# Performance work log

Hardware: AMD Instinct MI355X
Metric: run time of the kernel (lower is better)

Reference implementation:

```python
import jax, jax.numpy as jnp
import numpy as np

N_NODES = 100000
N_EDGES = 1200000
NFEAT = 64
NHID = 64
NCLASS = 16
BN_EPS = 1e-5
L2_EPS = 1e-12


def setup_inputs() -> dict:
    key = jax.random.key(0)
    ks = jax.random.split(key, 8)
    edge_index = jax.random.randint(ks[0], (2, N_EDGES), 0, N_NODES, dtype=jnp.int64)
    x = jax.random.normal(ks[1], (N_NODES, NFEAT), dtype=jnp.float32)
    # SAGEConv params: lin_l (neighbor path, has bias), lin_r (root path, no bias)
    W_l = jax.random.normal(ks[2], (NHID, NFEAT), dtype=jnp.float32) * (1.0 / np.sqrt(NFEAT))
    b_l = jnp.zeros((NHID,), dtype=jnp.float32)
    W_r = jax.random.normal(ks[3], (NHID, NFEAT), dtype=jnp.float32) * (1.0 / np.sqrt(NFEAT))
    # BatchNorm1d affine params
    gamma = jnp.ones((NHID,), dtype=jnp.float32)
    beta = jnp.zeros((NHID,), dtype=jnp.float32)
    # final fc (xavier-ish scale, zero bias per weights_init)
    W_fc = jax.random.normal(ks[4], (NCLASS, NHID), dtype=jnp.float32) * (1.0 / np.sqrt(NHID))
    b_fc = jnp.zeros((NCLASS,), dtype=jnp.float32)
    return {"edge_index": edge_index, "x": x, "W_l": W_l, "b_l": b_l,
            "W_r": W_r, "gamma": gamma, "beta": beta, "W_fc": W_fc, "b_fc": b_fc}


def reference(edge_index, x, W_l, b_l, W_r, gamma, beta, W_fc, b_fc):
    N = x.shape[0]
    src, dst = edge_index[0], edge_index[1]
    # SAGEConv mean aggregation: gather x at source nodes, scatter-mean to dst
    msgs = x[src]                                                  # [E, F]
    sums = jax.ops.segment_sum(msgs, dst, num_segments=N)         # [N, F]
    cnt = jax.ops.segment_sum(jnp.ones((src.shape[0], 1), x.dtype), dst, num_segments=N)
    mean = sums / jnp.maximum(cnt, 1.0)
    # out = lin_l(mean_neighbors) + lin_r(x_root)
    h = mean @ W_l.T + b_l + x @ W_r.T                              # [N, H]
    # normalize=True -> L2 normalize rows (F.normalize semantics)
    h = h / jnp.maximum(jnp.linalg.norm(h, axis=-1, keepdims=True), L2_EPS)
    # transition: ReLU -> BatchNorm1d (training stats) -> Dropout (identity in eval)
    h = jax.nn.relu(h)
    mu = jnp.mean(h, axis=0)
    var = jnp.var(h, axis=0)
    h = (h - mu) / jnp.sqrt(var + BN_EPS) * gamma + beta
    return h @ W_fc.T + b_fc                                        # [N, C]
```

## Files before the change

### kernel.cpp

```cpp
#include <hip/hip_runtime.h>
#include <hip/hip_bf16.h>


typedef __attribute__((ext_vector_type(8))) short short8;
typedef __attribute__((ext_vector_type(4))) float f32x4;

__device__ __forceinline__ unsigned short f2bf(float f) {
    unsigned int u = __builtin_bit_cast(unsigned int, f);
    u += 0x7FFFu + ((u >> 16) & 1u);
    return (unsigned short)(u >> 16);
}
__device__ __forceinline__ float bf2f(unsigned short s) {
    return __builtin_bit_cast(float, ((unsigned int)s) << 16);
}

#define CHUNK 8192

__device__ __forceinline__ int exclScan256(int v, int* swv) {
    const int t = threadIdx.x, lane = t & 63, wid = t >> 6;
    __syncthreads();
    int s = v;
#pragma unroll
    for (int off = 1; off < 64; off <<= 1) {
        int tt = __shfl_up(s, off);
        if (lane >= off) s += tt;
    }
    if (lane == 63) swv[wid] = s;
    __syncthreads();
    if (t == 0) {
        int a = 0;
#pragma unroll
        for (int w = 0; w < 4; ++w) { int tt = swv[w]; swv[w] = a; a += tt; }
    }
    __syncthreads();
    return s - v + swv[wid];
}

__global__ __launch_bounds__(256) void k_prep(const int* __restrict__ eidx,
                                              int* __restrict__ cnt,
                                              const float4* __restrict__ x4,
                                              ushort4* __restrict__ xbf,
                                              int E, int NB, int NBLK,
                                              int n4, int do_x) {
    __shared__ int lh[256];
    const int tid = threadIdx.x;
    if ((int)blockIdx.x < NBLK) {
        lh[tid] = 0;
        __syncthreads();
        const int base = blockIdx.x * CHUNK;
        for (int i = tid; i < CHUNK; i += 256) {
            int e = base + i;
            if (e < E) atomicAdd(&lh[eidx[E + e] >> 9], 1);
        }
        __syncthreads();
        if (tid < NB) cnt[(size_t)tid * NBLK + blockIdx.x] = lh[tid];
    } else if (do_x) {
        int t = ((int)blockIdx.x - NBLK) * 256 + tid;
        if (t < n4) {
            float4 v = x4[t];
            xbf[t] = make_ushort4(f2bf(v.x), f2bf(v.y), f2bf(v.z), f2bf(v.w));
        }
    }
}

__global__ __launch_bounds__(256) void k_scanbkt(int* __restrict__ cnt,
                                                 int* __restrict__ btot,
                                                 int NBLK) {
    __shared__ int swv[4];
    const int b = blockIdx.x;
    const int t = threadIdx.x;
    int v = (t < NBLK) ? cnt[(size_t)b * NBLK + t] : 0;
    int excl = exclScan256(v, swv);
    if (t < NBLK) cnt[(size_t)b * NBLK + t] = excl;
    if (t == 255) btot[b] = excl + v;
}

__global__ __launch_bounds__(256) void k_bscatter(const int* __restrict__ eidx,
                                                  const int* __restrict__ cnt,
                                                  const int* __restrict__ btot,
                                                  unsigned int* __restrict__ ebuf,
                                                  int E, int NB, int NBLK) {
    __shared__ int cur[256];
    __shared__ int swv[4];
    const int tid = threadIdx.x;
    int bv = (tid < NB) ? btot[tid] : 0;
    int bexcl = exclScan256(bv, swv);
    if (tid < NB)
        cur[tid] = bexcl + cnt[(size_t)tid * NBLK + blockIdx.x];
    __syncthreads();
    const int base = blockIdx.x * CHUNK;
    for (int i = tid; i < CHUNK; i += 256) {
        int e = base + i;
        if (e < E) {
            int d = eidx[E + e];
            int s = eidx[e];
            int p = atomicAdd(&cur[d >> 9], 1);
            ebuf[p] = (unsigned int)s | ((unsigned int)(d & 511) << 17);
        }
    }
}

__global__ __launch_bounds__(256) void k_bfinal(const unsigned int* __restrict__ ebuf,
                                                const int* __restrict__ btot,
                                                int* __restrict__ rowptr,
                                                int* __restrict__ colv,
                                                int N, int NB, int E) {
    __shared__ int h[512];
    __shared__ int swv[4];
    __shared__ int sseg[2];
    const int b = blockIdx.x;
    const int tid = threadIdx.x;
    int bv = (tid < NB) ? btot[tid] : 0;
    int bexcl = exclScan256(bv, swv);
    if (tid == b) { sseg[0] = bexcl; sseg[1] = bexcl + bv; }
    h[2 * tid] = 0;
    h[2 * tid + 1] = 0;
    __syncthreads();
    const int segb = sseg[0], sege = sseg[1];
    for (int i = segb + tid; i < sege; i += 256)
        atomicAdd(&h[ebuf[i] >> 17], 1);
    __syncthreads();
    int a0 = h[2 * tid], a1 = h[2 * tid + 1];
    int ts = a0 + a1;
    const int lane = tid & 63, wid = tid >> 6;
    int s = ts;
#pragma unroll
    for (int off = 1; off < 64; off <<= 1) {
        int tt = __shfl_up(s, off);
        if (lane >= off) s += tt;
    }
    if (lane == 63) swv[wid] = s;
    __syncthreads();
    if (tid == 0) {
        int a = 0;
#pragma unroll
        for (int w = 0; w < 4; ++w) { int tt = swv[w]; swv[w] = a; a += tt; }
    }
    __syncthreads();
    int excl = s - ts + swv[wid];
    h[2 * tid] = excl;
    h[2 * tid + 1] = excl + a0;
    int node = b * 512 + 2 * tid;
    if (node < N) rowptr[node] = segb + excl;
    if (node + 1 < N) rowptr[node + 1] = segb + excl + a0;
    __syncthreads();
    for (int i = segb + tid; i < sege; i += 256) {
        unsigned int u = ebuf[i];
        int p = atomicAdd(&h[u >> 17], 1);
        colv[segb + p] = (int)(u & 0x1FFFFu);
    }
    if (b == 0 && tid == 0) rowptr[N] = E;
}

__global__ __launch_bounds__(256) void k_gfused(
        const unsigned short* __restrict__ xbf,
        const int* __restrict__ rowptr, const int* __restrict__ colv,
        const float* __restrict__ Wl, const float* __restrict__ bl,
        const float* __restrict__ Wr,
        unsigned short* __restrict__ mh,
        float* __restrict__ pstats, int N) {
    __shared__ unsigned short sm[16][72];

    const int tid = threadIdx.x;
    const int tbase = blockIdx.x * 16;

    {
        const int nloc = tid >> 4;
        const int l = tid & 15;
        const int mrow = tbase + nloc;
        const int mld = (mrow < N) ? mrow : (N - 1);
        const uint2* xbf2 = (const uint2*)xbf;
        int b = rowptr[mld], e = rowptr[mld + 1];
        float a0 = 0.f, a1 = 0.f, a2 = 0.f, a3 = 0.f;
        int p = b;
        for (; p + 4 <= e; p += 4) {
            int s0 = colv[p], s1 = colv[p + 1], s2 = colv[p + 2], s3 = colv[p + 3];
            uint2 v0 = xbf2[(size_t)s0 * 16 + l];
            uint2 v1 = xbf2[(size_t)s1 * 16 + l];
            uint2 v2 = xbf2[(size_t)s2 * 16 + l];
            uint2 v3 = xbf2[(size_t)s3 * 16 + l];
            a0 += bf2f((unsigned short)(v0.x & 0xFFFF)) + bf2f((unsigned short)(v1.x & 0xFFFF)) +
                  bf2f((unsigned short)(v2.x & 0xFFFF)) + bf2f((unsigned short)(v3.x & 0xFFFF));
            a1 += bf2f((unsigned short)(v0.x >> 16)) + bf2f((unsigned short)(v1.x >> 16)) +
                  bf2f((unsigned short)(v2.x >> 16)) + bf2f((unsigned short)(v3.x >> 16));
            a2 += bf2f((unsigned short)(v0.y & 0xFFFF)) + bf2f((unsigned short)(v1.y & 0xFFFF)) +
                  bf2f((unsigned short)(v2.y & 0xFFFF)) + bf2f((unsigned short)(v3.y & 0xFFFF));
            a3 += bf2f((unsigned short)(v0.y >> 16)) + bf2f((unsigned short)(v1.y >> 16)) +
                  bf2f((unsigned short)(v2.y >> 16)) + bf2f((unsigned short)(v3.y >> 16));
        }
        for (; p < e; ++p) {
            int s0 = colv[p];
            uint2 v0 = xbf2[(size_t)s0 * 16 + l];
            a0 += bf2f((unsigned short)(v0.x & 0xFFFF));
            a1 += bf2f((unsigned short)(v0.x >> 16));
            a2 += bf2f((unsigned short)(v0.y & 0xFFFF));
            a3 += bf2f((unsigned short)(v0.y >> 16));
        }
        float inv = 1.0f / fmaxf((float)(e - b), 1.0f);
        *(ushort4*)&sm[nloc][l * 4] = make_ushort4(f2bf(a0 * inv), f2bf(a1 * inv),
                                                   f2bf(a2 * inv), f2bf(a3 * inv));
    }
    __syncthreads();
    if (tid >= 64) return;

    const int lane = tid;
    const int l15 = lane & 15;
    const int quad = lane >> 4;

    short8 afr[2], rfr[2];
    afr[0] = *(const short8*)&sm[l15][quad * 8];
    afr[1] = *(const short8*)&sm[l15][32 + quad * 8];
    const int rrow = tbase + l15;
    const int rld = (rrow < N) ? rrow : (N - 1);
    rfr[0] = *(const short8*)(xbf + (size_t)rld * 64 + quad * 8);
    rfr[1] = *(const short8*)(xbf + (size_t)rld * 64 + 32 + quad * 8);

    float blv[4];
#pragma unroll
    for (int f = 0; f < 4; ++f) blv[f] = bl[f * 16 + l15];

    f32x4 acc[4] = {{0.f, 0.f, 0.f, 0.f}, {0.f, 0.f, 0.f, 0.f},
                    {0.f, 0.f, 0.f, 0.f}, {0.f, 0.f, 0.f, 0.f}};
#pragma unroll
    for (int c = 0; c < 4; ++c) {
#pragma unroll
        for (int f = 0; f < 4; ++f) {
            const int n = f * 16 + l15;
            const float* wsrc = (c < 2)
                ? (Wl + (size_t)n * 64 + c * 32 + quad * 8)
                : (Wr + (size_t)n * 64 + (c - 2) * 32 + quad * 8);
            float4 w0 = *(const float4*)wsrc;
            float4 w1 = *(const float4*)(wsrc + 4);
            union { short8 v; unsigned short u[8]; } pk;
            pk.u[0] = f2bf(w0.x); pk.u[1] = f2bf(w0.y);
            pk.u[2] = f2bf(w0.z); pk.u[3] = f2bf(w0.w);
            pk.u[4] = f2bf(w1.x); pk.u[5] = f2bf(w1.y);
            pk.u[6] = f2bf(w1.z); pk.u[7] = f2bf(w1.w);
            acc[f] = __builtin_amdgcn_mfma_f32_16x16x32_bf16(
                (c < 2) ? afr[c] : rfr[c - 2], pk.v, acc[f], 0, 0, 0);
        }
    }

    float psum[4] = {0.f, 0.f, 0.f, 0.f};
    float psq[4] = {0.f, 0.f, 0.f, 0.f};
#pragma unroll
    for (int reg = 0; reg < 4; ++reg) {
        const int node = tbase + quad * 4 + reg;
        float hv[4];
        float ss = 0.f;
#pragma unroll
        for (int f = 0; f < 4; ++f) {
            hv[f] = acc[f][reg] + blv[f];
            ss += hv[f] * hv[f];
        }
        ss += __shfl_xor(ss, 1);
        ss += __shfl_xor(ss, 2);
        ss += __shfl_xor(ss, 4);
        ss += __shfl_xor(ss, 8);
        float sc = 1.0f / fmaxf(sqrtf(ss), 1e-12f);
        if (node < N) {
#pragma unroll
            for (int f = 0; f < 4; ++f) {
                float r = fmaxf(hv[f] * sc, 0.f);
                unsigned short rb = f2bf(r);
                float e = bf2f(rb);
                mh[(size_t)node * 64 + f * 16 + l15] = rb;
                psum[f] += e;
                psq[f] += e * e;
            }
        }
    }

#pragma unroll
    for (int f = 0; f < 4; ++f) {
        psum[f] += __shfl_xor(psum[f], 16);
        psum[f] += __shfl_xor(psum[f], 32);
        psq[f] += __shfl_xor(psq[f], 16);
        psq[f] += __shfl_xor(psq[f], 32);
    }
    if (lane < 16) {
#pragma unroll
        for (int f = 0; f < 4; ++f) {
            pstats[(size_t)blockIdx.x * 128 + f * 16 + l15] = psum[f];
            pstats[(size_t)blockIdx.x * 128 + 64 + f * 16 + l15] = psq[f];
        }
    }
}

__global__ __launch_bounds__(256) void k_gather_f32(
        const float4* __restrict__ x4, const int* __restrict__ rowptr,
        const int* __restrict__ colv, ushort4* __restrict__ mh, int N) {
    int t = blockIdx.x * 256 + threadIdx.x;
    int n = t >> 4;
    int l = t & 15;
    if (n >= N) return;
    int b = rowptr[n], e = rowptr[n + 1];
    float ax = 0.f, ay = 0.f, az = 0.f, aw = 0.f;
    int p = b;
    for (; p + 4 <= e; p += 4) {
        int s0 = colv[p], s1 = colv[p + 1], s2 = colv[p + 2], s3 = colv[p + 3];
        float4 v0 = x4[(size_t)s0 * 16 + l];
        float4 v1 = x4[(size_t)s1 * 16 + l];
        float4 v2 = x4[(size_t)s2 * 16 + l];
        float4 v3 = x4[(size_t)s3 * 16 + l];
        ax += (v0.x + v1.x) + (v2.x + v3.x);
        ay += (v0.y + v1.y) + (v2.y + v3.y);
        az += (v0.z + v1.z) + (v2.z + v3.z);
        aw += (v0.w + v1.w) + (v2.w + v3.w);
    }
    for (; p < e; ++p) {
        int s0 = colv[p];
        float4 v0 = x4[(size_t)s0 * 16 + l];
        ax += v0.x; ay += v0.y; az += v0.z; aw += v0.w;
    }
    float inv = 1.0f / fmaxf((float)(e - b), 1.0f);
    mh[(size_t)n * 16 + l] = make_ushort4(f2bf(ax * inv), f2bf(ay * inv),
                                          f2bf(az * inv), f2bf(aw * inv));
}

__global__ __launch_bounds__(256) void k_fused_legacy(
        const float* __restrict__ x,
        const float* __restrict__ Wl, const float* __restrict__ bl,
        const float* __restrict__ Wr,
        unsigned short* __restrict__ mh,
        float* __restrict__ pstats, int N) {
    __shared__ float sRed[4][128];
    const int tid = threadIdx.x;
    const int wid = tid >> 6;
    const int lane = tid & 63;
    const int l15 = lane & 15;
    const int quad = lane >> 4;

    short8 bfrag[4][4];
#pragma unroll
    for (int c = 0; c < 4; ++c) {
#pragma unroll
        for (int f = 0; f < 4; ++f) {
            const int n = f * 16 + l15;
            const float* wsrc = (c < 2)
                ? (Wl + (size_t)n * 64 + c * 32 + quad * 8)
                : (Wr + (size_t)n * 64 + (c - 2) * 32 + quad * 8);
            float4 w0 = *(const float4*)wsrc;
            float4 w1 = *(const float4*)(wsrc + 4);
            union { short8 v; unsigned short u[8]; } pk;
            pk.u[0] = f2bf(w0.x); pk.u[1] = f2bf(w0.y);
            pk.u[2] = f2bf(w0.z); pk.u[3] = f2bf(w0.w);
            pk.u[4] = f2bf(w1.x); pk.u[5] = f2bf(w1.y);
            pk.u[6] = f2bf(w1.z); pk.u[7] = f2bf(w1.w);
            bfrag[c][f] = pk.v;
        }
    }
    float blv[4];
#pragma unroll
    for (int f = 0; f < 4; ++f) blv[f] = bl[f * 16 + l15];

    const int tbase = blockIdx.x * 64 + wid * 16;
    const int mrow = tbase + l15;
    const int mld = (mrow < N) ? mrow : (N - 1);
    f32x4 acc[4] = {{0.f, 0.f, 0.f, 0.f}, {0.f, 0.f, 0.f, 0.f},
                    {0.f, 0.f, 0.f, 0.f}, {0.f, 0.f, 0.f, 0.f}};
#pragma unroll
    for (int c = 0; c < 2; ++c) {
        short8 a = *(const short8*)(mh + (size_t)mld * 64 + c * 32 + quad * 8);
#pragma unroll
        for (int f = 0; f < 4; ++f)
            acc[f] = __builtin_amdgcn_mfma_f32_16x16x32_bf16(a, bfrag[c][f], acc[f], 0, 0, 0);
    }
#pragma unroll
    for (int c = 0; c < 2; ++c) {
        const float* xp = x + (size_t)mld * 64 + c * 32 + quad * 8;
        float4 a0 = *(const float4*)xp;
        float4 a1 = *(const float4*)(xp + 4);
        union { short8 v; unsigned short u[8]; } pk;
        pk.u[0] = f2bf(a0.x); pk.u[1] = f2bf(a0.y);
        pk.u[2] = f2bf(a0.z); pk.u[3] = f2bf(a0.w);
        pk.u[4] = f2bf(a1.x); pk.u[5] = f2bf(a1.y);
        pk.u[6] = f2bf(a1.z); pk.u[7] = f2bf(a1.w);
#pragma unroll
        for (int f = 0; f < 4; ++f)
            acc[f] = __builtin_amdgcn_mfma_f32_16x16x32_bf16(pk.v, bfrag[c + 2][f], acc[f], 0, 0, 0);
    }

    float psum[4] = {0.f, 0.f, 0.f, 0.f};
    float psq[4] = {0.f, 0.f, 0.f, 0.f};
#pragma unroll
    for (int reg = 0; reg < 4; ++reg) {
        const int node = tbase + quad * 4 + reg;
        float hv[4];
        float ss = 0.f;
#pragma unroll
        for (int f = 0; f < 4; ++f) {
            hv[f] = acc[f][reg] + blv[f];
            ss += hv[f] * hv[f];
        }
        ss += __shfl_xor(ss, 1);
        ss += __shfl_xor(ss, 2);
        ss += __shfl_xor(ss, 4);
        ss += __shfl_xor(ss, 8);
        float sc = 1.0f / fmaxf(sqrtf(ss), 1e-12f);
        if (node < N) {
#pragma unroll
            for (int f = 0; f < 4; ++f) {
                float r = fmaxf(hv[f] * sc, 0.f);
                unsigned short rb = f2bf(r);
                float e = bf2f(rb);
                mh[(size_t)node * 64 + f * 16 + l15] = rb;
                psum[f] += e;
                psq[f] += e * e;
            }
        }
    }
#pragma unroll
    for (int f = 0; f < 4; ++f) {
        psum[f] += __shfl_xor(psum[f], 16);
        psum[f] += __shfl_xor(psum[f], 32);
        psq[f] += __shfl_xor(psq[f], 16);
        psq[f] += __shfl_xor(psq[f], 32);
    }
    if (lane < 16) {
#pragma unroll
        for (int f = 0; f < 4; ++f) {
            sRed[wid][f * 16 + l15] = psum[f];
            sRed[wid][64 + f * 16 + l15] = psq[f];
        }
    }
    __syncthreads();
    if (tid < 128) {
        float v = sRed[0][tid] + sRed[1][tid] + sRed[2][tid] + sRed[3][tid];
        pstats[(size_t)blockIdx.x * 128 + tid] = v;
    }
}

__global__ __launch_bounds__(64) void k_stats(const float* __restrict__ pstats,
                                              float* __restrict__ stats, int nblk) {
    int col = blockIdx.x;
    int l = threadIdx.x;
    float s = 0.f;
    for (int r = l; r < nblk; r += 64) s += pstats[(size_t)r * 128 + col];
    s += __shfl_xor(s, 1);
    s += __shfl_xor(s, 2);
    s += __shfl_xor(s, 4);
    s += __shfl_xor(s, 8);
    s += __shfl_xor(s, 16);
    s += __shfl_xor(s, 32);
    if (l == 0) stats[col] = s;
}

__global__ __launch_bounds__(256) void k_out(
        const unsigned short* __restrict__ h, const float* __restrict__ stats,
        const float* __restrict__ gamma, const float* __restrict__ beta,
        const float* __restrict__ Wfc, const float* __restrict__ bfc,
        float* __restrict__ out, int N) {
    __shared__ float sWm[64 * 16];
    __shared__ float sShift[64];
    __shared__ float sBase[16];
    const int tid = threadIdx.x;
    const float invN = 1.0f / (float)N;
    if (tid < 64) {
        float mu = stats[tid] * invN;
        float var = stats[64 + tid] * invN - mu * mu;
        float sc = gamma[tid] / sqrtf(var + 1e-5f);
        sShift[tid] = beta[tid] - mu * sc;
#pragma unroll
        for (int c = 0; c < 16; ++c) sWm[tid * 16 + c] = Wfc[c * 64 + tid] * sc;
    }
    __syncthreads();
    if (tid < 16) {
        float b = bfc[tid];
#pragma unroll
        for (int j = 0; j < 64; ++j) b += sShift[j] * Wfc[tid * 64 + j];
        sBase[tid] = b;
    }
    __syncthreads();
    int g = blockIdx.x * 256 + tid;
    int n = g >> 4;
    int c = g & 15;
    if (n >= N) return;
    const ushort4* h4 = (const ushort4*)(h + (size_t)n * 64);
    float acc = sBase[c];
#pragma unroll
    for (int jq = 0; jq < 16; ++jq) {
        ushort4 v = h4[jq];
        acc += bf2f(v.x) * sWm[(jq * 4 + 0) * 16 + c];
        acc += bf2f(v.y) * sWm[(jq * 4 + 1) * 16 + c];
        acc += bf2f(v.z) * sWm[(jq * 4 + 2) * 16 + c];
        acc += bf2f(v.w) * sWm[(jq * 4 + 3) * 16 + c];
    }
    out[(size_t)n * 16 + c] = acc;
}

extern "C" void kernel_launch(void* const* d_in, const int* in_sizes, int n_in,
                              void* d_out, int out_size, void* d_ws, size_t ws_size,
                              hipStream_t stream) {
    const int* eidx = (const int*)d_in[0];
    const float* x = (const float*)d_in[1];
    const float* Wl = (const float*)d_in[2];
    const float* bl = (const float*)d_in[3];
    const float* Wr = (const float*)d_in[4];
    const float* gamma = (const float*)d_in[5];
    const float* beta = (const float*)d_in[6];
    const float* Wfc = (const float*)d_in[7];
    const float* bfc = (const float*)d_in[8];
    float* out = (float*)d_out;

    const int E = in_sizes[0] / 2;
    const int N = in_sizes[1] / 64;
    const int NB = (N + 511) >> 9;
    const int NBLK = (E + CHUNK - 1) / CHUNK;
    const int fbG = (N + 15) / 16;
    const int fbL = (N + 63) / 64;
    const int n4 = N * 16;

    int* cnt = (int*)d_ws;
    int* btot = cnt + (size_t)NB * NBLK;
    int* rowptr = btot + NB;
    float* pstats = (float*)(rowptr + N + 1);
    float* stats = pstats + (size_t)fbG * 128;
    int* colv = (int*)(stats + 128);
    unsigned int* ebuf = (unsigned int*)(colv + E);
    unsigned short* mh = (unsigned short*)(((uintptr_t)(ebuf + E) + 15) & ~(uintptr_t)15);
    unsigned short* xbf = mh + (size_t)N * 64;

    size_t need_bf = (size_t)((char*)(xbf + (size_t)N * 64) - (char*)d_ws);
    const int use_bf = (ws_size >= need_bf) ? 1 : 0;

    int cbl = use_bf ? (n4 + 255) / 256 : 0;
    k_prep<<<NBLK + cbl, 256, 0, stream>>>(eidx, cnt, (const float4*)x,
                                           (ushort4*)xbf, E, NB, NBLK, n4, use_bf);
    k_scanbkt<<<NB, 256, 0, stream>>>(cnt, btot, NBLK);
    k_bscatter<<<NBLK, 256, 0, stream>>>(eidx, cnt, btot, ebuf, E, NB, NBLK);
    k_bfinal<<<NB, 256, 0, stream>>>(ebuf, btot, rowptr, colv, N, NB, E);

    if (use_bf) {
        k_gfused<<<fbG, 256, 0, stream>>>(xbf, rowptr, colv, Wl, bl, Wr,
                                          mh, pstats, N);
        k_stats<<<128, 64, 0, stream>>>(pstats, stats, fbG);
    } else {
        int gblocks = (int)(((size_t)N * 16 + 255) / 256);
        k_gather_f32<<<gblocks, 256, 0, stream>>>((const float4*)x, rowptr, colv,
                                                  (ushort4*)mh, N);
        k_fused_legacy<<<fbL, 256, 0, stream>>>(x, Wl, bl, Wr, mh, pstats, N);
        k_stats<<<128, 64, 0, stream>>>(pstats, stats, fbL);
    }

    int oblocks = (int)(((size_t)N * 16 + 255) / 256);
    k_out<<<oblocks, 256, 0, stream>>>(mh, stats, gamma, beta, Wfc, bfc, out, N);
}
```

Before: 245.3 us.

## Split fused GEMM epilogue across all four wavefronts by output column tile

The MFMA projection stage after the neighbor gather previously ran on a single wavefront, leaving three of four waves idle. Each wave now computes one 16-column tile of the 64-wide output. The per-row L2 norm is assembled through a small shared-memory buffer and an extra barrier, and BN partial stats are written per column. This spreads weight conversion and MFMA work across the block, in exchange for a block-wide sync and redundant loads of the A fragments by every wave.

```diff
diff --git a/kernel.cpp b/kernel.cpp
--- a/kernel.cpp
+++ b/kernel.cpp
@@ -160,6 +160,7 @@
         unsigned short* __restrict__ mh,
         float* __restrict__ pstats, int N) {
     __shared__ unsigned short sm[16][72];
+    __shared__ float ssS[16][4];
 
     const int tid = threadIdx.x;
     const int tbase = blockIdx.x * 16;
@@ -201,11 +202,12 @@
                                                    f2bf(a2 * inv), f2bf(a3 * inv));
     }
     __syncthreads();
-    if (tid >= 64) return;
-
-    const int lane = tid;
+
+    const int wid = tid >> 6;
+    const int lane = tid & 63;
     const int l15 = lane & 15;
     const int quad = lane >> 4;
+    const int n = wid * 16 + l15;
 
     short8 afr[2], rfr[2];
     afr[0] = *(const short8*)&sm[l15][quad * 8];
@@ -215,75 +217,61 @@
     rfr[0] = *(const short8*)(xbf + (size_t)rld * 64 + quad * 8);
     rfr[1] = *(const short8*)(xbf + (size_t)rld * 64 + 32 + quad * 8);
 
-    float blv[4];
-#pragma unroll
-    for (int f = 0; f < 4; ++f) blv[f] = bl[f * 16 + l15];
-
-    f32x4 acc[4] = {{0.f, 0.f, 0.f, 0.f}, {0.f, 0.f, 0.f, 0.f},
-                    {0.f, 0.f, 0.f, 0.f}, {0.f, 0.f, 0.f, 0.f}};
+    const float blv = bl[n];
+
+    f32x4 acc = {0.f, 0.f, 0.f, 0.f};
 #pragma unroll
     for (int c = 0; c < 4; ++c) {
-#pragma unroll
-        for (int f = 0; f < 4; ++f) {
-            const int n = f * 16 + l15;
-            const float* wsrc = (c < 2)
-                ? (Wl + (size_t)n * 64 + c * 32 + quad * 8)
-                : (Wr + (size_t)n * 64 + (c - 2) * 32 + quad * 8);
-            float4 w0 = *(const float4*)wsrc;
-            float4 w1 = *(const float4*)(wsrc + 4);
-            union { short8 v; unsigned short u[8]; } pk;
-            pk.u[0] = f2bf(w0.x); pk.u[1] = f2bf(w0.y);
-            pk.u[2] = f2bf(w0.z); pk.u[3] = f2bf(w0.w);
-            pk.u[4] = f2bf(w1.x); pk.u[5] = f2bf(w1.y);
-            pk.u[6] = f2bf(w1.z); pk.u[7] = f2bf(w1.w);
-            acc[f] = __builtin_amdgcn_mfma_f32_16x16x32_bf16(
-                (c < 2) ? afr[c] : rfr[c - 2], pk.v, acc[f], 0, 0, 0);
-        }
-    }
-
-    float psum[4] = {0.f, 0.f, 0.f, 0.f};
-    float psq[4] = {0.f, 0.f, 0.f, 0.f};
+        const float* wsrc = (c < 2)
+            ? (Wl + (size_t)n * 64 + c * 32 + quad * 8)
+            : (Wr + (size_t)n * 64 + (c - 2) * 32 + quad * 8);
+        float4 w0 = *(const float4*)wsrc;
+        float4 w1 = *(const float4*)(wsrc + 4);
+        union { short8 v; unsigned short u[8]; } pk;
+        pk.u[0] = f2bf(w0.x); pk.u[1] = f2bf(w0.y);
+        pk.u[2] = f2bf(w0.z); pk.u[3] = f2bf(w0.w);
+        pk.u[4] = f2bf(w1.x); pk.u[5] = f2bf(w1.y);
+        pk.u[6] = f2bf(w1.z); pk.u[7] = f2bf(w1.w);
+        acc = __builtin_amdgcn_mfma_f32_16x16x32_bf16(
+            (c < 2) ? afr[c] : rfr[c - 2], pk.v, acc, 0, 0, 0);
+    }
+
+    float hv[4];
+#pragma unroll
+    for (int reg = 0; reg < 4; ++reg) {
+        hv[reg] = acc[reg] + blv;
+        float ssp = hv[reg] * hv[reg];
+        ssp += __shfl_xor(ssp, 1);
+        ssp += __shfl_xor(ssp, 2);
+        ssp += __shfl_xor(ssp, 4);
+        ssp += __shfl_xor(ssp, 8);
+        if (l15 == 0) ssS[quad * 4 + reg][wid] = ssp;
+    }
+    __syncthreads();
+
+    float psum = 0.f, psq = 0.f;
 #pragma unroll
     for (int reg = 0; reg < 4; ++reg) {
         const int node = tbase + quad * 4 + reg;
-        float hv[4];
-        float ss = 0.f;
-#pragma unroll
-        for (int f = 0; f < 4; ++f) {
-            hv[f] = acc[f][reg] + blv[f];
-            ss += hv[f] * hv[f];
-        }
-        ss += __shfl_xor(ss, 1);
-        ss += __shfl_xor(ss, 2);
-        ss += __shfl_xor(ss, 4);
-        ss += __shfl_xor(ss, 8);
+        float4 sv = *(const float4*)ssS[quad * 4 + reg];
+        float ss = (sv.x + sv.y) + (sv.z + sv.w);
         float sc = 1.0f / fmaxf(sqrtf(ss), 1e-12f);
         if (node < N) {
-#pragma unroll
-            for (int f = 0; f < 4; ++f) {
-                float r = fmaxf(hv[f] * sc, 0.f);
-                unsigned short rb = f2bf(r);
-                float e = bf2f(rb);
-                mh[(size_t)node * 64 + f * 16 + l15] = rb;
-                psum[f] += e;
-                psq[f] += e * e;
-            }
-        }
-    }
-
-#pragma unroll
-    for (int f = 0; f < 4; ++f) {
-        psum[f] += __shfl_xor(psum[f], 16);
-        psum[f] += __shfl_xor(psum[f], 32);
-        psq[f] += __shfl_xor(psq[f], 16);
-        psq[f] += __shfl_xor(psq[f], 32);
-    }
-    if (lane < 16) {
-#pragma unroll
-        for (int f = 0; f < 4; ++f) {
-            pstats[(size_t)blockIdx.x * 128 + f * 16 + l15] = psum[f];
-            pstats[(size_t)blockIdx.x * 128 + 64 + f * 16 + l15] = psq[f];
-        }
+            float r = fmaxf(hv[reg] * sc, 0.f);
+            unsigned short rb = f2bf(r);
+            float e = bf2f(rb);
+            mh[(size_t)node * 64 + n] = rb;
+            psum += e;
+            psq += e * e;
+        }
+    }
+    psum += __shfl_xor(psum, 16);
+    psum += __shfl_xor(psum, 32);
+    psq += __shfl_xor(psq, 16);
+    psq += __shfl_xor(psq, 32);
+    if (quad == 0) {
+        pstats[(size_t)blockIdx.x * 128 + n] = psum;
+        pstats[(size_t)blockIdx.x * 128 + 64 + n] = psq;
     }
 }
 
```

After: 250.0 us. No clear change (+1.9%).
